# Kernel tuning notes

Measured on AMD Instinct MI355X. Metric: run time of the kernel, lower is better.

## Reference

```python
import jax, jax.numpy as jnp
import numpy as np

D_MODEL = 1024
D_HEAD = 64

def setup_inputs() -> dict:
    key = jax.random.key(0)
    kx, kk, kq, kv = jax.random.split(key, 4)
    s = D_MODEL ** -0.5
    return {
        "x": jax.random.normal(kx, (4, 4096, D_MODEL), dtype=jnp.float32),
        "Wk": jax.random.normal(kk, (D_MODEL, D_HEAD), dtype=jnp.float32) * s,
        "Wq": jax.random.normal(kq, (D_MODEL, D_HEAD), dtype=jnp.float32) * s,
        "Wv": jax.random.normal(kv, (D_MODEL, D_HEAD), dtype=jnp.float32) * s,
    }

def reference(x, Wk, Wq, Wv):
    # x: [B, T, d_model]; Wk/Wq/Wv: [d_model, d_head]
    B, T, _ = x.shape
    d_head = Wk.shape[1]
    k = x @ Wk  # [B, T, d_head]
    q = x @ Wq
    v = x @ Wv
    scores = jnp.einsum("btd,bsd->bts", q, k) * (d_head ** -0.5)  # [B, T, T]
    causal = jnp.tril(jnp.ones((T, T), dtype=bool))
    scores = jnp.where(causal, scores, -jnp.inf)
    weights = jax.nn.softmax(scores, axis=-1)
    return jnp.einsum("bts,bsd->btd", weights, v)
```

## Files before the change

kernel.cpp:

```cpp
#include <hip/hip_runtime.h>

typedef __attribute__((ext_vector_type(8))) short bf16x8;
typedef __attribute__((ext_vector_type(4))) float f32x4;

#define DI __device__ __forceinline__

DI unsigned short f2bf(float f) {
    unsigned int u = __builtin_bit_cast(unsigned int, f);
    u += 0x7fff + ((u >> 16) & 1);
    return (unsigned short)(u >> 16);
}

DI unsigned int cvtpk(float lo, float hi) {
    unsigned int r;
    asm("v_cvt_pk_bf16_f32 %0, %1, %2" : "=v"(r) : "v"(lo), "v"(hi));
    return r;
}

DI void gl_lds16(const void* g, void* l) {
    __builtin_amdgcn_global_load_lds(
        (const __attribute__((address_space(1))) unsigned int*)g,
        (__attribute__((address_space(3))) unsigned int*)l, 16, 0, 0);
}

#define WAITCNT(n) asm volatile("s_waitcnt vmcnt(" #n ")" ::: "memory")

__global__ __launch_bounds__(256) void wt_kernel(
    const float* __restrict__ Wk, const float* __restrict__ Wq,
    const float* __restrict__ Wv, unsigned short* __restrict__ Wt)
{
    __shared__ float ws[64][65];
    const int m = blockIdx.x >> 4, kc = blockIdx.x & 15;
    const float* W = (m == 0) ? Wq : (m == 1) ? Wk : Wv;
    const float scale = (m == 0) ? 0.18033688011112042f : 1.0f;
    const int tid = threadIdx.x;
    #pragma unroll
    for (int r = 0; r < 16; ++r) {
        int idx = r * 256 + tid;
        ws[idx >> 6][idx & 63] = W[(kc * 64 + (idx >> 6)) * 64 + (idx & 63)] * scale;
    }
    __syncthreads();
    const int c = tid >> 2, k4 = (tid & 3) * 16;
    bf16x8 o0, o1;
    #pragma unroll
    for (int j = 0; j < 8; ++j) o0[j] = (short)f2bf(ws[k4 + j][c]);
    #pragma unroll
    for (int j = 0; j < 8; ++j) o1[j] = (short)f2bf(ws[k4 + 8 + j][c]);
    unsigned short* dst = Wt + ((size_t)m * 64 + c) * 1024 + kc * 64 + k4;
    *(bf16x8*)dst = o0;
    *(bf16x8*)(dst + 8) = o1;
}

__global__ __launch_bounds__(256) void proj_kernel(
    const float* __restrict__ x, const unsigned short* __restrict__ Wt,
    unsigned short* __restrict__ qw, unsigned short* __restrict__ kw,
    unsigned short* __restrict__ vT)
{
    __shared__ char LDSx[3][8192];
    __shared__ char LDSb[3][6144];

    const int tid = threadIdx.x;
    const int w = tid >> 6, l = tid & 63;
    const int xr = l & 15, lg = l >> 4;
    const int rb = blockIdx.x & 255, ch = blockIdx.x >> 8;
    const int row0 = rb * 64;

    const char* xsrc = (const char*)x + (size_t)row0 * 4096;
    const char* Wtb = (const char*)Wt;

    const int xrow_l = l >> 3, xcb = (l & 7) * 16;
    const int brow_l = l >> 2, bcb = (l & 3) * 16;

    auto stage = [&](int nb, int s) {
        #pragma unroll
        for (int c = 0; c < 4; ++c) {
            const int ci = w + 4 * c;
            if (ci < 8) {
                const int row = ci * 8 + xrow_l;
                const int sw = (row & 7) << 4;
                gl_lds16(xsrc + (size_t)row * 4096 + (size_t)s * 128 + (xcb ^ sw),
                         LDSx[nb] + ci * 1024);
            } else if (ci < 14) {
                const int c8 = ci - 8;
                const int r = c8 * 16 + brow_l;
                const int sw = ((r >> 1) & 3) << 4;
                const int wtrow = (r >> 5) * 64 + ch * 32 + (r & 31);
                gl_lds16(Wtb + (size_t)wtrow * 2048 + (size_t)s * 64 + (bcb ^ sw),
                         LDSb[nb] + c8 * 1024);
            }
        }
    };

    f32x4 acc[3][2];
    #pragma unroll
    for (int m = 0; m < 3; ++m)
        #pragma unroll
        for (int tt = 0; tt < 2; ++tt) { f32x4 z = {0.f,0.f,0.f,0.f}; acc[m][tt] = z; }

    const int Rw = w * 16 + xr;
    const int swx = (Rw & 7) << 4;

    auto compute = [&](int pb) {
        float4 va = *(const float4*)(LDSx[pb] + Rw * 128 + ((32 * lg) ^ swx));
        float4 vb = *(const float4*)(LDSx[pb] + Rw * 128 + ((32 * lg + 16) ^ swx));
        bf16x8 a;
        a[0] = (short)f2bf(va.x); a[1] = (short)f2bf(va.y);
        a[2] = (short)f2bf(va.z); a[3] = (short)f2bf(va.w);
        a[4] = (short)f2bf(vb.x); a[5] = (short)f2bf(vb.y);
        a[6] = (short)f2bf(vb.z); a[7] = (short)f2bf(vb.w);
        __builtin_amdgcn_s_setprio(1);
        #pragma unroll
        for (int m = 0; m < 3; ++m)
            #pragma unroll
            for (int tt = 0; tt < 2; ++tt) {
                const int rB = m * 32 + tt * 16 + xr;
                bf16x8 bfr = *(const bf16x8*)(LDSb[pb] + rB * 64 +
                                ((16 * lg) ^ (((rB >> 1) & 3) << 4)));
                acc[m][tt] = __builtin_amdgcn_mfma_f32_16x16x32_bf16(a, bfr, acc[m][tt], 0, 0, 0);
            }
        __builtin_amdgcn_s_setprio(0);
    };

    stage(0, 0); stage(1, 1);

    int cb = 0, nb = 2;
    for (int s = 0; s < 32; ++s) {
        if (s == 31) { WAITCNT(0); }
        else if (w < 2) { WAITCNT(4); }
        else { WAITCNT(3); }
        __builtin_amdgcn_sched_barrier(0);
        __builtin_amdgcn_s_barrier();
        if (s + 2 < 32) stage(nb, s + 2);
        compute(cb);
        cb = (cb == 2) ? 0 : cb + 1;
        nb = (nb == 2) ? 0 : nb + 1;
    }

    const int bb = row0 >> 12;
    #pragma unroll
    for (int tt = 0; tt < 2; ++tt) {
        const int col = ch * 32 + tt * 16 + xr;
        unsigned short pv4[4];
        #pragma unroll
        for (int i = 0; i < 4; ++i) {
            const int grow = row0 + w * 16 + 4 * lg + i;
            qw[(size_t)grow * 64 + col] = f2bf(acc[0][tt][i]);
            kw[(size_t)grow * 64 + col] = f2bf(acc[1][tt][i]);
            pv4[i] = f2bf(acc[2][tt][i]);
        }
        const int lr0 = (row0 & 4095) + w * 16 + 4 * lg;
        *(uint2*)&vT[((size_t)bb * 64 + col) * 4096 + lr0] = *(const uint2*)pv4;
    }
}

__global__ __launch_bounds__(256) void attn_kernel(
    const unsigned short* __restrict__ qw, const unsigned short* __restrict__ kw,
    const unsigned short* __restrict__ vT,
    unsigned short* __restrict__ POb, float* __restrict__ Pl)
{
    __shared__ __align__(16) unsigned short Kb[2][4096];
    __shared__ __align__(16) unsigned short Vb[2][4096];
    __shared__ __align__(16) unsigned short Ps[4][2][16][32];

    const int id = blockIdx.x;
    const int qb = 63 - (id & 63);
    const int b  = (id >> 6) & 3;
    const int c  = id >> 8;
    if (c * 8 > qb) return;

    const int tid = threadIdx.x;
    const int w = tid >> 6, l = tid & 63;
    const int xr = l & 15, g = l >> 4;
    const int rw = w >> 1;
    const int kw2 = w & 1;

    const int t0 = c * 8;
    const int rem0 = qb + 1 - t0;
    const int tcnt = rem0 < 8 ? rem0 : 8;
    const size_t base = (size_t)b * 4096;
    const int qrow0 = qb * 64 + rw * 32;
    const int myrowA = qrow0 + xr;
    const int myrowB = qrow0 + 16 + xr;

    bf16x8 aqA[2], aqB[2];
    #pragma unroll
    for (int h = 0; h < 2; ++h) {
        aqA[h] = *(const bf16x8*)(qw + (base + myrowA) * 64 + 32 * h + 8 * g);
        aqB[h] = *(const bf16x8*)(qw + (base + myrowB) * 64 + 32 * h + 8 * g);
    }

    const int wo0 = w * 2048, wo1 = wo0 + 1024;
    const int o0 = wo0 + 16 * l, o1 = wo1 + 16 * l;
    const int k0sw = (o0 & ~127) | ((o0 & 127) ^ (((o0 >> 7) & 7) << 4));
    const int k1sw = (o1 & ~127) | ((o1 & 127) ^ (((o1 >> 7) & 7) << 4));
    const size_t v0sw = (size_t)(o0 >> 7) * 8192 + ((o0 & 127) ^ (((o0 >> 7) & 7) << 4));
    const size_t v1sw = (size_t)(o1 >> 7) * 8192 + ((o1 & 127) ^ (((o1 >> 7) & 7) << 4));
    const char* kwb  = (const char*)kw + base * 128;
    const char* vtb0 = (const char*)vT + (size_t)b * 64 * 8192;

    auto stage = [&](int bi, int it) {
        const char* kt = kwb + (size_t)it * 8192;
        gl_lds16(kt + k0sw, (char*)Kb[bi] + wo0);
        gl_lds16(kt + k1sw, (char*)Kb[bi] + wo1);
        const char* vt = vtb0 + (size_t)it * 128;
        gl_lds16(vt + v0sw, (char*)Vb[bi] + wo0);
        gl_lds16(vt + v1sw, (char*)Vb[bi] + wo1);
    };

    f32x4 accO[2][4];
    #pragma unroll
    for (int gr = 0; gr < 2; ++gr)
        #pragma unroll
        for (int t = 0; t < 4; ++t) { f32x4 z = {0.f,0.f,0.f,0.f}; accO[gr][t] = z; }
    float lsA = 0.f, lsB = 0.f;

    const int swz = (xr & 7) << 4;
    const int swzP = (xr & 3) << 4;
    char* const psrowA = (char*)Ps + w * 2048 + xr * 64;
    char* const psrowB = psrowA + 1024;

    stage(0, t0);
    if (tcnt > 1) stage(1, t0 + 1);

    for (int tt = 0; tt < tcnt; ++tt) {
        const int it = t0 + tt;
        const int bi = tt & 1;
        if (tt + 1 < tcnt) { WAITCNT(4); } else { WAITCNT(0); }
        __builtin_amdgcn_sched_barrier(0);
        __builtin_amdgcn_s_barrier();

        const char* kbase = (const char*)Kb[bi] + kw2 * 4096;
        f32x4 sA[2], sB[2];
        __builtin_amdgcn_s_setprio(1);
        #pragma unroll
        for (int t = 0; t < 2; ++t) {
            f32x4 z = {0.f,0.f,0.f,0.f};
            sA[t] = z; sB[t] = z;
            #pragma unroll
            for (int h = 0; h < 2; ++h) {
                bf16x8 ak = *(const bf16x8*)(kbase + (16 * t + xr) * 128 + ((64 * h + 16 * g) ^ swz));
                sA[t] = __builtin_amdgcn_mfma_f32_16x16x32_bf16(ak, aqA[h], sA[t], 0, 0, 0);
                sB[t] = __builtin_amdgcn_mfma_f32_16x16x32_bf16(ak, aqB[h], sB[t], 0, 0, 0);
            }
        }
        __builtin_amdgcn_s_setprio(0);

        if (it == qb) {
            #pragma unroll
            for (int t = 0; t < 2; ++t)
                #pragma unroll
                for (int i = 0; i < 4; ++i) {
                    const int key = it * 64 + kw2 * 32 + 16 * t + 4 * g + i;
                    if (key > myrowA) sA[t][i] = -1e30f;
                    if (key > myrowB) sB[t][i] = -1e30f;
                }
        }

        #pragma unroll
        for (int t = 0; t < 2; ++t)
            #pragma unroll
            for (int i = 0; i < 4; ++i) {
                sA[t][i] = exp2f(sA[t][i]);
                sB[t][i] = exp2f(sB[t][i]);
            }
        lsA += ((sA[0][0] + sA[0][1]) + (sA[0][2] + sA[0][3]))
             + ((sA[1][0] + sA[1][1]) + (sA[1][2] + sA[1][3]));
        lsB += ((sB[0][0] + sB[0][1]) + (sB[0][2] + sB[0][3]))
             + ((sB[1][0] + sB[1][1]) + (sB[1][2] + sB[1][3]));

        #pragma unroll
        for (int t = 0; t < 2; ++t) {
            uint2 uA, uB;
            uA.x = cvtpk(sA[t][0], sA[t][1]); uA.y = cvtpk(sA[t][2], sA[t][3]);
            uB.x = cvtpk(sB[t][0], sB[t][1]); uB.y = cvtpk(sB[t][2], sB[t][3]);
            *(uint2*)(psrowA + ((32 * t + 8 * g) ^ swzP)) = uA;
            *(uint2*)(psrowB + ((32 * t + 8 * g) ^ swzP)) = uB;
        }
        bf16x8 paA = *(const bf16x8*)(psrowA + ((16 * g) ^ swzP));
        bf16x8 paB = *(const bf16x8*)(psrowB + ((16 * g) ^ swzP));

        const char* vbase = (const char*)Vb[bi];
        __builtin_amdgcn_s_setprio(1);
        #pragma unroll
        for (int t = 0; t < 4; ++t) {
            bf16x8 av = *(const bf16x8*)(vbase + (16 * t + xr) * 128 + ((kw2 * 64 + 16 * g) ^ swz));
            accO[0][t] = __builtin_amdgcn_mfma_f32_16x16x32_bf16(av, paA, accO[0][t], 0, 0, 0);
            accO[1][t] = __builtin_amdgcn_mfma_f32_16x16x32_bf16(av, paB, accO[1][t], 0, 0, 0);
        }
        __builtin_amdgcn_s_setprio(0);

        __builtin_amdgcn_s_barrier();
        if (tt + 2 < tcnt) stage(bi, it + 2);
    }

    lsA += __shfl_xor(lsA, 16, 64); lsA += __shfl_xor(lsA, 32, 64);
    lsB += __shfl_xor(lsB, 16, 64); lsB += __shfl_xor(lsB, 32, 64);

    __syncthreads();
    float* scr  = (float*)Kb;
    float* scrL = (float*)Vb;
    if (kw2) {
        #pragma unroll
        for (int gr = 0; gr < 2; ++gr)
            #pragma unroll
            for (int t = 0; t < 4; ++t)
                *(f32x4*)(scr + rw * 2048 + (gr * 4 + t) * 256 + g * 64 + xr * 4) = accO[gr][t];
        if (l < 16) {
            scrL[rw * 128 + l] = lsA;
            scrL[rw * 128 + 16 + l] = lsB;
        }
    }
    __syncthreads();
    if (!kw2) {
        const size_t prow = (size_t)(b * 8 + c) * 4096 + qb * 64 + rw * 32;
        #pragma unroll
        for (int gr = 0; gr < 2; ++gr)
            #pragma unroll
            for (int t = 0; t < 4; ++t) {
                f32x4 o = accO[gr][t] + *(const f32x4*)(scr + rw * 2048 + (gr * 4 + t) * 256 + g * 64 + xr * 4);
                uint2 uu;
                uu.x = cvtpk(o[0], o[1]);
                uu.y = cvtpk(o[2], o[3]);
                *(uint2*)&POb[(prow + gr * 16 + xr) * 64 + 16 * t + 4 * g] = uu;
            }
        if (l < 16) {
            Pl[prow + l]      = lsA + scrL[rw * 128 + l];
            Pl[prow + 16 + l] = lsB + scrL[rw * 128 + 16 + l];
        }
    }
}

__global__ __launch_bounds__(256) void merge_kernel(
    const unsigned short* __restrict__ POb, const float* __restrict__ Pl,
    float* __restrict__ out)
{
    const int gid = blockIdx.x * 256 + threadIdx.x;
    const int r = gid >> 2;
    const int c0 = (gid & 3) * 16;
    const int b = r >> 12, lr = r & 4095;
    const int nc = (lr >> 9) + 1;

    float L = 0.f;
    #pragma unroll
    for (int ci = 0; ci < 8; ++ci)
        if (ci < nc) L += Pl[(size_t)(b * 8 + ci) * 4096 + lr];
    const float rL = 1.0f / L;

    float acc[16];
    #pragma unroll
    for (int j = 0; j < 16; ++j) acc[j] = 0.f;

    #pragma unroll
    for (int ci = 0; ci < 8; ++ci) {
        if (ci < nc) {
            const unsigned short* p = POb + ((size_t)(b * 8 + ci) * 4096 + lr) * 64 + c0;
            uint4 u0 = *(const uint4*)p;
            uint4 u1 = *(const uint4*)(p + 8);
            const unsigned int us[8] = {u0.x, u0.y, u0.z, u0.w, u1.x, u1.y, u1.z, u1.w};
            #pragma unroll
            for (int k = 0; k < 8; ++k) {
                acc[2 * k]     += __builtin_bit_cast(float, us[k] << 16);
                acc[2 * k + 1] += __builtin_bit_cast(float, us[k] & 0xFFFF0000u);
            }
        }
    }
    float* op = out + (size_t)r * 64 + c0;
    #pragma unroll
    for (int j = 0; j < 4; ++j) {
        float4 v;
        v.x = acc[4 * j]     * rL;
        v.y = acc[4 * j + 1] * rL;
        v.z = acc[4 * j + 2] * rL;
        v.w = acc[4 * j + 3] * rL;
        *(float4*)(op + 4 * j) = v;
    }
}

extern "C" void kernel_launch(void* const* d_in, const int* in_sizes, int n_in,
                              void* d_out, int out_size, void* d_ws, size_t ws_size,
                              hipStream_t stream) {
    const float* x  = (const float*)d_in[0];
    const float* Wk = (const float*)d_in[1];
    const float* Wq = (const float*)d_in[2];
    const float* Wv = (const float*)d_in[3];
    float* out = (float*)d_out;

    char* wsb = (char*)d_ws;
    unsigned short* POb = (unsigned short*)wsb;
    float* Pl = (float*)(wsb + (size_t)17 * 1024 * 1024);
    unsigned short* Wt = (unsigned short*)(wsb + (size_t)24 * 1024 * 1024);
    unsigned short* qw = Wt + (size_t)3 * 64 * 1024;
    unsigned short* kw = qw + (size_t)16384 * 64;
    unsigned short* vT = kw + (size_t)16384 * 64;

    hipLaunchKernelGGL(wt_kernel, dim3(48), dim3(256), 0, stream, Wk, Wq, Wv, Wt);
    hipLaunchKernelGGL(proj_kernel, dim3(512), dim3(256), 0, stream, x, Wt, qw, kw, vT);
    hipLaunchKernelGGL(attn_kernel, dim3(2048), dim3(256), 0, stream, qw, kw, vT, POb, Pl);
    hipLaunchKernelGGL(merge_kernel, dim3(256), dim3(256), 0, stream, POb, Pl, out);
}
```

Baseline: 67.31 us.

## Use 128-row query tiles per block with each wave covering full key tile

Query tiles per block grow from 64 to 128 rows, so each of four waves owns 32 query rows and processes all 64 keys per tile, instead of pairs of waves splitting keys. This removes the end-of-kernel LDS reduction between the two key halves and roughly halves the number of blocks, so each staged K/V tile is reused by twice as many queries. The trade-offs are more registers per wave, fewer blocks to fill the GPU, and masked wasted work on the diagonal since the mask now spans two key tiles per query block.

```diff
diff --git a/kernel.cpp b/kernel.cpp
--- a/kernel.cpp
+++ b/kernel.cpp
@@ -160,25 +160,24 @@
 {
     __shared__ __align__(16) unsigned short Kb[2][4096];
     __shared__ __align__(16) unsigned short Vb[2][4096];
-    __shared__ __align__(16) unsigned short Ps[4][2][16][32];
+    __shared__ __align__(16) unsigned short Ps[4][32][64];
 
     const int id = blockIdx.x;
-    const int qb = 63 - (id & 63);
-    const int b  = (id >> 6) & 3;
-    const int c  = id >> 8;
-    if (c * 8 > qb) return;
+    const int qb = 31 - (id & 31);
+    const int b  = (id >> 5) & 3;
+    const int c  = id >> 7;
+    if (c * 4 > qb) return;
 
     const int tid = threadIdx.x;
     const int w = tid >> 6, l = tid & 63;
     const int xr = l & 15, g = l >> 4;
-    const int rw = w >> 1;
-    const int kw2 = w & 1;
 
     const int t0 = c * 8;
-    const int rem0 = qb + 1 - t0;
+    const int nt = 2 * qb + 2;
+    const int rem0 = nt - t0;
     const int tcnt = rem0 < 8 ? rem0 : 8;
     const size_t base = (size_t)b * 4096;
-    const int qrow0 = qb * 64 + rw * 32;
+    const int qrow0 = qb * 128 + w * 32;
     const int myrowA = qrow0 + xr;
     const int myrowB = qrow0 + 16 + xr;
 
@@ -207,17 +206,17 @@
         gl_lds16(vt + v1sw, (char*)Vb[bi] + wo1);
     };
 
-    f32x4 accO[2][4];
-    #pragma unroll
-    for (int gr = 0; gr < 2; ++gr)
-        #pragma unroll
-        for (int t = 0; t < 4; ++t) { f32x4 z = {0.f,0.f,0.f,0.f}; accO[gr][t] = z; }
+    f32x4 accA[4], accB[4];
+    #pragma unroll
+    for (int t = 0; t < 4; ++t) {
+        f32x4 z = {0.f,0.f,0.f,0.f};
+        accA[t] = z; accB[t] = z;
+    }
     float lsA = 0.f, lsB = 0.f;
 
     const int swz = (xr & 7) << 4;
-    const int swzP = (xr & 3) << 4;
-    char* const psrowA = (char*)Ps + w * 2048 + xr * 64;
-    char* const psrowB = psrowA + 1024;
+    char* const psrowA = (char*)Ps + w * 4096 + xr * 128;
+    char* const psrowB = psrowA + 2048;
 
     stage(0, t0);
     if (tcnt > 1) stage(1, t0 + 1);
@@ -229,64 +228,74 @@
         __builtin_amdgcn_sched_barrier(0);
         __builtin_amdgcn_s_barrier();
 
-        const char* kbase = (const char*)Kb[bi] + kw2 * 4096;
-        f32x4 sA[2], sB[2];
+        const char* kbase = (const char*)Kb[bi];
+        f32x4 sA[4], sB[4];
         __builtin_amdgcn_s_setprio(1);
         #pragma unroll
-        for (int t = 0; t < 2; ++t) {
+        for (int t = 0; t < 4; ++t) {
             f32x4 z = {0.f,0.f,0.f,0.f};
             sA[t] = z; sB[t] = z;
             #pragma unroll
             for (int h = 0; h < 2; ++h) {
-                bf16x8 ak = *(const bf16x8*)(kbase + (16 * t + xr) * 128 + ((64 * h + 16 * g) ^ swz));
+                bf16x8 ak = *(const bf16x8*)(kbase + (xr + 16 * t) * 128 + ((64 * h + 16 * g) ^ swz));
                 sA[t] = __builtin_amdgcn_mfma_f32_16x16x32_bf16(ak, aqA[h], sA[t], 0, 0, 0);
                 sB[t] = __builtin_amdgcn_mfma_f32_16x16x32_bf16(ak, aqB[h], sB[t], 0, 0, 0);
             }
         }
         __builtin_amdgcn_s_setprio(0);
 
-        if (it == qb) {
-            #pragma unroll
-            for (int t = 0; t < 2; ++t)
+        if (it >= 2 * qb) {
+            #pragma unroll
+            for (int t = 0; t < 4; ++t)
                 #pragma unroll
                 for (int i = 0; i < 4; ++i) {
-                    const int key = it * 64 + kw2 * 32 + 16 * t + 4 * g + i;
+                    const int key = it * 64 + 16 * t + 4 * g + i;
                     if (key > myrowA) sA[t][i] = -1e30f;
                     if (key > myrowB) sB[t][i] = -1e30f;
                 }
         }
 
         #pragma unroll
-        for (int t = 0; t < 2; ++t)
+        for (int t = 0; t < 4; ++t)
             #pragma unroll
             for (int i = 0; i < 4; ++i) {
                 sA[t][i] = exp2f(sA[t][i]);
                 sB[t][i] = exp2f(sB[t][i]);
             }
         lsA += ((sA[0][0] + sA[0][1]) + (sA[0][2] + sA[0][3]))
-             + ((sA[1][0] + sA[1][1]) + (sA[1][2] + sA[1][3]));
+             + ((sA[1][0] + sA[1][1]) + (sA[1][2] + sA[1][3]))
+             + ((sA[2][0] + sA[2][1]) + (sA[2][2] + sA[2][3]))
+             + ((sA[3][0] + sA[3][1]) + (sA[3][2] + sA[3][3]));
         lsB += ((sB[0][0] + sB[0][1]) + (sB[0][2] + sB[0][3]))
-             + ((sB[1][0] + sB[1][1]) + (sB[1][2] + sB[1][3]));
-
-        #pragma unroll
-        for (int t = 0; t < 2; ++t) {
+             + ((sB[1][0] + sB[1][1]) + (sB[1][2] + sB[1][3]))
+             + ((sB[2][0] + sB[2][1]) + (sB[2][2] + sB[2][3]))
+             + ((sB[3][0] + sB[3][1]) + (sB[3][2] + sB[3][3]));
+
+        #pragma unroll
+        for (int t = 0; t < 4; ++t) {
             uint2 uA, uB;
             uA.x = cvtpk(sA[t][0], sA[t][1]); uA.y = cvtpk(sA[t][2], sA[t][3]);
             uB.x = cvtpk(sB[t][0], sB[t][1]); uB.y = cvtpk(sB[t][2], sB[t][3]);
-            *(uint2*)(psrowA + ((32 * t + 8 * g) ^ swzP)) = uA;
-            *(uint2*)(psrowB + ((32 * t + 8 * g) ^ swzP)) = uB;
-        }
-        bf16x8 paA = *(const bf16x8*)(psrowA + ((16 * g) ^ swzP));
-        bf16x8 paB = *(const bf16x8*)(psrowB + ((16 * g) ^ swzP));
-
+            *(uint2*)(psrowA + ((32 * t + 8 * g) ^ swz)) = uA;
+            *(uint2*)(psrowB + ((32 * t + 8 * g) ^ swz)) = uB;
+        }
+
+        bf16x8 paA[2], paB[2];
+        #pragma unroll
+        for (int h = 0; h < 2; ++h) {
+            paA[h] = *(const bf16x8*)(psrowA + ((16 * g + 64 * h) ^ swz));
+            paB[h] = *(const bf16x8*)(psrowB + ((16 * g + 64 * h) ^ swz));
+        }
         const char* vbase = (const char*)Vb[bi];
         __builtin_amdgcn_s_setprio(1);
         #pragma unroll
-        for (int t = 0; t < 4; ++t) {
-            bf16x8 av = *(const bf16x8*)(vbase + (16 * t + xr) * 128 + ((kw2 * 64 + 16 * g) ^ swz));
-            accO[0][t] = __builtin_amdgcn_mfma_f32_16x16x32_bf16(av, paA, accO[0][t], 0, 0, 0);
-            accO[1][t] = __builtin_amdgcn_mfma_f32_16x16x32_bf16(av, paB, accO[1][t], 0, 0, 0);
-        }
+        for (int t = 0; t < 4; ++t)
+            #pragma unroll
+            for (int h = 0; h < 2; ++h) {
+                bf16x8 av = *(const bf16x8*)(vbase + (16 * t + xr) * 128 + ((64 * h + 16 * g) ^ swz));
+                accA[t] = __builtin_amdgcn_mfma_f32_16x16x32_bf16(av, paA[h], accA[t], 0, 0, 0);
+                accB[t] = __builtin_amdgcn_mfma_f32_16x16x32_bf16(av, paB[h], accB[t], 0, 0, 0);
+            }
         __builtin_amdgcn_s_setprio(0);
 
         __builtin_amdgcn_s_barrier();
@@ -296,37 +305,18 @@
     lsA += __shfl_xor(lsA, 16, 64); lsA += __shfl_xor(lsA, 32, 64);
     lsB += __shfl_xor(lsB, 16, 64); lsB += __shfl_xor(lsB, 32, 64);
 
-    __syncthreads();
-    float* scr  = (float*)Kb;
-    float* scrL = (float*)Vb;
-    if (kw2) {
-        #pragma unroll
-        for (int gr = 0; gr < 2; ++gr)
-            #pragma unroll
-            for (int t = 0; t < 4; ++t)
-                *(f32x4*)(scr + rw * 2048 + (gr * 4 + t) * 256 + g * 64 + xr * 4) = accO[gr][t];
-        if (l < 16) {
-            scrL[rw * 128 + l] = lsA;
-            scrL[rw * 128 + 16 + l] = lsB;
-        }
-    }
-    __syncthreads();
-    if (!kw2) {
-        const size_t prow = (size_t)(b * 8 + c) * 4096 + qb * 64 + rw * 32;
-        #pragma unroll
-        for (int gr = 0; gr < 2; ++gr)
-            #pragma unroll
-            for (int t = 0; t < 4; ++t) {
-                f32x4 o = accO[gr][t] + *(const f32x4*)(scr + rw * 2048 + (gr * 4 + t) * 256 + g * 64 + xr * 4);
-                uint2 uu;
-                uu.x = cvtpk(o[0], o[1]);
-                uu.y = cvtpk(o[2], o[3]);
-                *(uint2*)&POb[(prow + gr * 16 + xr) * 64 + 16 * t + 4 * g] = uu;
-            }
-        if (l < 16) {
-            Pl[prow + l]      = lsA + scrL[rw * 128 + l];
-            Pl[prow + 16 + l] = lsB + scrL[rw * 128 + 16 + l];
-        }
+    const size_t prow = (size_t)(b * 8 + c) * 4096 + qrow0;
+    #pragma unroll
+    for (int t = 0; t < 4; ++t) {
+        uint2 uA, uB;
+        uA.x = cvtpk(accA[t][0], accA[t][1]); uA.y = cvtpk(accA[t][2], accA[t][3]);
+        uB.x = cvtpk(accB[t][0], accB[t][1]); uB.y = cvtpk(accB[t][2], accB[t][3]);
+        *(uint2*)&POb[(prow + xr) * 64 + 16 * t + 4 * g] = uA;
+        *(uint2*)&POb[(prow + 16 + xr) * 64 + 16 * t + 4 * g] = uB;
+    }
+    if (l < 16) {
+        Pl[prow + l]      = lsA;
+        Pl[prow + 16 + l] = lsB;
     }
 }
 
@@ -395,6 +385,6 @@
 
     hipLaunchKernelGGL(wt_kernel, dim3(48), dim3(256), 0, stream, Wk, Wq, Wv, Wt);
     hipLaunchKernelGGL(proj_kernel, dim3(512), dim3(256), 0, stream, x, Wt, qw, kw, vT);
-    hipLaunchKernelGGL(attn_kernel, dim3(2048), dim3(256), 0, stream, qw, kw, vT, POb, Pl);
+    hipLaunchKernelGGL(attn_kernel, dim3(1024), dim3(256), 0, stream, qw, kw, vT, POb, Pl);
     hipLaunchKernelGGL(merge_kernel, dim3(256), dim3(256), 0, stream, POb, Pl, out);
 }
```

Result: slower. 74.76 us (+11.1%).
